# Kernel optimization log

Measured on AMD Instinct MI355X. Metric: run time of the kernel, lower is better.

## Reference

```python
import jax, jax.numpy as jnp
import numpy as np


def setup_inputs() -> dict:
    key = jax.random.key(0)
    B, F = 16384, 4096
    x = jax.random.normal(key, (B, F), dtype=jnp.float32)
    return {"x": x, "k": 64}


def reference(x, k):
    # top-k along dim=1 (last axis for 2D input)
    _, idx = jax.lax.top_k(x, k)                      # idx: [B, k]
    B = x.shape[0]
    rows = jnp.arange(B)[:, None]                     # [B, 1]
    mask = jnp.zeros_like(x).at[rows, idx].set(1.0)   # scatter ones at top-k positions
    return x * mask
```

## Files before the change

kernel.cpp:

```cpp
#include <hip/hip_runtime.h>
#include <stdint.h>

#define TK_F       4096
#define TK_THREADS 256
#define TK_EPT     16
#define TK_NBINS   2048
#define TK_HSLOTS  (TK_NBINS + (TK_NBINS >> 5))
#define TK_CAP     256

__device__ __forceinline__ unsigned int tk_f2u(unsigned int b) {
    return b ^ ((unsigned int)(((int)b) >> 31) | 0x80000000u);
}
__device__ __forceinline__ unsigned int tk_u2f(unsigned int u) {
    return u ^ ((~(unsigned int)(((int)u) >> 31)) | 0x80000000u);
}
__device__ __forceinline__ unsigned int tk_slot(unsigned int b) {
    return b + (b >> 5);
}

__global__ __launch_bounds__(TK_THREADS, 8)
void tk_topk_mask(const float* __restrict__ x, const int* __restrict__ kp,
                  float* __restrict__ out, int B)
{
    __shared__ unsigned int hist[TK_HSLOTS];
    __shared__ unsigned int cand[TK_CAP];
    __shared__ unsigned int waveTot[TK_THREADS / 64];
    __shared__ unsigned int sh_cnt;
    __shared__ int          sh_b;
    __shared__ unsigned int sh_cum;
    __shared__ unsigned int sh_T, sh_g, sh_e;

    const int tid = threadIdx.x;
    const int row = blockIdx.x;
    if (row >= B) return;
    const unsigned int k = (unsigned int)kp[0];

    const unsigned int* xr   = (const unsigned int*)(x + (size_t)row * TK_F);
    unsigned int*       orow = (unsigned int*)(out + (size_t)row * TK_F);
    const uint4*        xv   = (const uint4*)xr;

    unsigned int u[TK_EPT];
    #pragma unroll
    for (int v = 0; v < 4; ++v) {
        uint4 q = xv[tid + v * TK_THREADS];
        u[v*4+0] = tk_f2u(q.x);
        u[v*4+1] = tk_f2u(q.y);
        u[v*4+2] = tk_f2u(q.z);
        u[v*4+3] = tk_f2u(q.w);
    }

    #pragma unroll
    for (int i = 0; i < 8; ++i) hist[tid + i * TK_THREADS] = 0u;
    if (tid < TK_HSLOTS - 8 * TK_THREADS) hist[8 * TK_THREADS + tid] = 0u;
    if (tid == 0) { sh_cnt = 0u; sh_b = -1; }
    __syncthreads();

    #pragma unroll
    for (int e = 0; e < TK_EPT; ++e)
        atomicAdd(&hist[tk_slot(u[e] >> 21)], 1u);
    __syncthreads();

    unsigned int hbin[8];
    unsigned int s = 0;
    const unsigned int sbase = tk_slot((unsigned int)tid * 8u);
    #pragma unroll
    for (int j = 0; j < 8; ++j) { hbin[j] = hist[sbase + j]; s += hbin[j]; }

    unsigned int acc = s;
    const int lane = tid & 63;
    #pragma unroll
    for (int d = 1; d < 64; d <<= 1) {
        unsigned int v = (unsigned int)__shfl_down((int)acc, d, 64);
        if (lane + d < 64) acc += v;
    }
    const int wid = tid >> 6;
    if (lane == 0) waveTot[wid] = acc;
    __syncthreads();
    unsigned int later = 0;
    #pragma unroll
    for (int w = 0; w < TK_THREADS / 64; ++w)
        if (w > wid) later += waveTot[w];

    unsigned int run = later + (acc - s);
    #pragma unroll
    for (int j = 7; j >= 0; --j) {
        unsigned int h = hbin[j];
        if (run < k && run + h >= k) { sh_b = tid * 8 + j; sh_cum = run; }
        run += h;
    }
    __syncthreads();

    const int b = sh_b;
    if (b < 0) {
        #pragma unroll
        for (int v = 0; v < 4; ++v) {
            uint4 q;
            q.x = tk_u2f(u[v*4+0]); q.y = tk_u2f(u[v*4+1]);
            q.z = tk_u2f(u[v*4+2]); q.w = tk_u2f(u[v*4+3]);
            ((uint4*)orow)[tid + v * TK_THREADS] = q;
        }
        return;
    }
    const unsigned int cum = sh_cum;

    #pragma unroll
    for (int e = 0; e < TK_EPT; ++e) {
        if ((int)(u[e] >> 21) == b) {
            unsigned int p = atomicAdd(&sh_cnt, 1u);
            if (p < TK_CAP) cand[p] = u[e];
        }
    }
    __syncthreads();

    const unsigned int L = (sh_cnt < TK_CAP) ? sh_cnt : TK_CAP;
    const unsigned int r = k - cum;
    for (unsigned int j = tid; j < L; j += TK_THREADS) {
        unsigned int uj = cand[j];
        unsigned int g = 0, eq = 0;
        for (unsigned int i = 0; i < L; ++i) {
            unsigned int ui = cand[i];
            g  += (ui > uj)  ? 1u : 0u;
            eq += (ui == uj) ? 1u : 0u;
        }
        if (g < r && g + eq >= r) { sh_T = uj; sh_g = g; sh_e = eq; }
    }
    __syncthreads();

    const unsigned int T  = sh_T;
    const unsigned int re = r - sh_g;
    const unsigned int ce = sh_e;
    const bool easy = (ce == re);

    #pragma unroll
    for (int v = 0; v < 4; ++v) {
        uint4 q;
        #pragma unroll
        for (int j = 0; j < 4; ++j) {
            unsigned int uu  = u[v*4+j];
            unsigned int val = 0u;
            if (uu > T) {
                val = tk_u2f(uu);
            } else if (uu == T) {
                if (easy) {
                    val = tk_u2f(uu);
                } else {
                    int idx = (tid + v * TK_THREADS) * 4 + j;
                    unsigned int cnt = 0;
                    for (int i = 0; i < idx; ++i)
                        cnt += (tk_f2u(xr[i]) == T) ? 1u : 0u;
                    if (cnt < re) val = tk_u2f(uu);
                }
            }
            (&q.x)[j] = val;
        }
        ((uint4*)orow)[tid + v * TK_THREADS] = q;
    }
}

extern "C" void kernel_launch(void* const* d_in, const int* in_sizes, int n_in,
                              void* d_out, int out_size, void* d_ws, size_t ws_size,
                              hipStream_t stream) {
    const float* x   = (const float*)d_in[0];
    const int*   kp  = (const int*)d_in[1];
    float*       out = (float*)d_out;
    const int B = in_sizes[0] / TK_F;
    hipLaunchKernelGGL(tk_topk_mask, dim3(B), dim3(TK_THREADS), 0, stream,
                       x, kp, out, B);
}
```

Measured before the change: 527.9 us.

## Process 16 rows per persistent block with double-buffered register prefetch

Each block now handles 16 rows, alternating two register buffers so the next-next row's global load is issued while the current row is being selected. Barriers are replaced by a lighter lgkmcnt-wait plus s_barrier, the histogram is reset with vector stores, and candidate appends are aggregated per thread to cut LDS atomics. The goal is to hide HBM load latency behind the histogram and selection work. In exchange the grid is 16x smaller (1024 blocks), the register budget is higher, and launch bounds are lowered to 4 blocks per CU, which may reduce occupancy.

```diff
diff --git a/kernel.cpp b/kernel.cpp
--- a/kernel.cpp
+++ b/kernel.cpp
@@ -3,7 +3,7 @@
 
 #define TK_F       4096
 #define TK_THREADS 256
-#define TK_EPT     16
+#define TK_R       16
 #define TK_NBINS   2048
 #define TK_HSLOTS  (TK_NBINS + (TK_NBINS >> 5))
 #define TK_CAP     256
@@ -18,142 +18,198 @@
     return b + (b >> 5);
 }
 
-__global__ __launch_bounds__(TK_THREADS, 8)
+#define TK_BAR() do {                                          \
+    asm volatile("s_waitcnt lgkmcnt(0)" ::: "memory");         \
+    __builtin_amdgcn_s_barrier();                              \
+    asm volatile("" ::: "memory");                             \
+} while (0)
+
+#define TK_BODY(U, RR) do {                                                         \
+    const int  row = rowBase + (RR);                                                \
+    const bool rv  = (row < B);                                                     \
+    const size_t rbase = (size_t)(rv ? row : (B - 1)) * TK_F;                       \
+            \
+    _Pragma("unroll")                                                               \
+    for (int e = 0; e < 16; ++e) {                                                  \
+        const unsigned int uu = tk_f2u(U[e]);                                       \
+        U[e] = uu;                                                                  \
+        atomicAdd(&hist[tk_slot(uu >> 21)], 1u);                                    \
+    }                                                                               \
+    TK_BAR();                                           \
+                             \
+    unsigned int hbin[8]; unsigned int s = 0;                                       \
+    { const unsigned int sb = tk_slot((unsigned int)tid * 8u);                      \
+      _Pragma("unroll")                                                             \
+      for (int j = 0; j < 8; ++j) { hbin[j] = hist[sb + j]; s += hbin[j]; } }       \
+    unsigned int acc = s;                                                           \
+    _Pragma("unroll")                                                               \
+    for (int d = 1; d < 64; d <<= 1) {                                              \
+        const unsigned int t_ = (unsigned int)__shfl_down((int)acc, d, 64);         \
+        if (lane + d < 64) acc += t_;                                               \
+    }                                                                               \
+    if (lane == 0) ((unsigned int*)&waveTotV)[wid] = acc;                           \
+    TK_BAR();                                          \
+    { const uint4 wt = waveTotV;                                                    \
+      unsigned int later = 0;                                                       \
+      if (wid < 3) later += wt.w;                                                   \
+      if (wid < 2) later += wt.z;                                                   \
+      if (wid < 1) later += wt.y;                                                   \
+      unsigned int run = later + (acc - s);                                         \
+      _Pragma("unroll")                                                             \
+      for (int j = 7; j >= 0; --j) {                                                \
+          const unsigned int h = hbin[j];                                           \
+          if (run < k && run + h >= k) { sh_b = tid * 8 + j; sh_cum = run; }        \
+          run += h;                                                                 \
+      }                                                                             \
+      if (tid == 0) sh_cnt = 0u;  \
+    }                                                                               \
+    TK_BAR();                          \
+    {                                                                               \
+      const int          bb  = sh_b;                                                \
+      const unsigned int cum = sh_cum;                                              \
+                     \
+      unsigned int c0 = 0, c1 = 0, nm = 0;                                          \
+      _Pragma("unroll")                                                             \
+      for (int e = 0; e < 16; ++e) {                                                \
+          const unsigned int uu = U[e];                                             \
+          if ((int)(uu >> 21) == bb) {                                              \
+              if (nm == 0u) c0 = uu;                                                \
+              else if (nm == 1u) c1 = uu;                                           \
+              else { const unsigned int p = atomicAdd(&sh_cnt, 1u);                 \
+                     if (p < TK_CAP) cand[p] = uu; }                                \
+              ++nm;                                                                 \
+          }                                                                         \
+      }                                                                             \
+      if (nm) {                                                                     \
+          const unsigned int take = nm < 2u ? nm : 2u;                              \
+          const unsigned int p0 = atomicAdd(&sh_cnt, take);                         \
+          if (p0 < TK_CAP) cand[p0] = c0;                                           \
+          if (take > 1u && p0 + 1u < TK_CAP) cand[p0 + 1u] = c1;                    \
+      }                                                                             \
+               \
+      const uint4 z4 = make_uint4(0u, 0u, 0u, 0u);                                  \
+      hist4[tid] = z4; hist4[tid + 256] = z4;                                       \
+      if (tid < (TK_HSLOTS / 4 - 512)) hist4[512 + tid] = z4;                       \
+      TK_BAR();                          \
+      const unsigned int L  = sh_cnt < TK_CAP ? sh_cnt : TK_CAP;                    \
+      const unsigned int rk = k - cum;                                              \
+      for (unsigned int j = (unsigned int)tid; j < L; j += TK_THREADS) {            \
+          const unsigned int uj = cand[j];                                          \
+          unsigned int g = 0, eq = 0;                                               \
+          for (unsigned int i = 0; i < L; ++i) {                                    \
+              const unsigned int ui = cand[i];                                      \
+              g  += (ui > uj)  ? 1u : 0u;                                           \
+              eq += (ui == uj) ? 1u : 0u;                                           \
+          }                                                                         \
+          if (g < rk && g + eq >= rk) { sh_T = uj; sh_g = g; sh_e = eq; }           \
+      }                                                                             \
+      TK_BAR();                                          \
+      const unsigned int T  = sh_T;                                                 \
+      const unsigned int re = rk - sh_g;                                            \
+      const bool easy = (sh_e == re);                                               \
+      unsigned int*       orow = (unsigned int*)(out + rbase);                      \
+      const unsigned int* xr   = (const unsigned int*)(x + rbase);                  \
+      _Pragma("unroll")                                                             \
+      for (int v = 0; v < 4; ++v) {                                                 \
+          uint4 q;                                                                  \
+          _Pragma("unroll")                                                         \
+          for (int j = 0; j < 4; ++j) {                                             \
+              const unsigned int uu = U[v*4 + j];                                   \
+              unsigned int val = 0u;                                                \
+              if (uu > T) {                                                         \
+                  val = tk_u2f(uu);                                                 \
+              } else if (uu == T) {                                                 \
+                  if (easy) { val = tk_u2f(uu); }                                   \
+                  else {                                                            \
+                             \
+                      const int idx = (tid + v * TK_THREADS) * 4 + j;               \
+                      unsigned int c2 = 0;                                          \
+                      for (int i = 0; i < idx; ++i)                                 \
+                          c2 += (tk_f2u(xr[i]) == T) ? 1u : 0u;                     \
+                      if (c2 < re) val = tk_u2f(uu);                                \
+                  }                                                                 \
+              }                                                                     \
+              (&q.x)[j] = val;                                                      \
+          }                                                                         \
+          if (rv) ((uint4*)orow)[tid + v * TK_THREADS] = q;                         \
+      }                                                                             \
+            \
+      if ((RR) + 2 < TK_R) {                                                        \
+          int prow = rowBase + (RR) + 2; if (prow >= B) prow = B - 1;               \
+          const uint4* pv = (const uint4*)(x + (size_t)prow * TK_F);                \
+          _Pragma("unroll")                                                         \
+          for (int v = 0; v < 4; ++v) {                                             \
+              const uint4 q = pv[tid + v * TK_THREADS];                             \
+              U[v*4+0] = q.x; U[v*4+1] = q.y; U[v*4+2] = q.z; U[v*4+3] = q.w;       \
+          }                                                                         \
+      }                                                                             \
+    }                                                                               \
+} while (0)
+
+__global__ __launch_bounds__(TK_THREADS, 4)
 void tk_topk_mask(const float* __restrict__ x, const int* __restrict__ kp,
                   float* __restrict__ out, int B)
 {
-    __shared__ unsigned int hist[TK_HSLOTS];
+    __shared__ uint4        hist4[TK_HSLOTS / 4];
     __shared__ unsigned int cand[TK_CAP];
-    __shared__ unsigned int waveTot[TK_THREADS / 64];
+    __shared__ uint4        waveTotV;
     __shared__ unsigned int sh_cnt;
     __shared__ int          sh_b;
-    __shared__ unsigned int sh_cum;
-    __shared__ unsigned int sh_T, sh_g, sh_e;
-
-    const int tid = threadIdx.x;
-    const int row = blockIdx.x;
-    if (row >= B) return;
+    __shared__ unsigned int sh_cum, sh_T, sh_g, sh_e;
+
+    const int tid  = (int)threadIdx.x;
+    const int lane = tid & 63;
+    const int wid  = tid >> 6;
+    const int rowBase = (int)blockIdx.x * TK_R;
+    if (rowBase >= B) return;
     const unsigned int k = (unsigned int)kp[0];
-
-    const unsigned int* xr   = (const unsigned int*)(x + (size_t)row * TK_F);
-    unsigned int*       orow = (unsigned int*)(out + (size_t)row * TK_F);
-    const uint4*        xv   = (const uint4*)xr;
-
-    unsigned int u[TK_EPT];
-    #pragma unroll
-    for (int v = 0; v < 4; ++v) {
-        uint4 q = xv[tid + v * TK_THREADS];
-        u[v*4+0] = tk_f2u(q.x);
-        u[v*4+1] = tk_f2u(q.y);
-        u[v*4+2] = tk_f2u(q.z);
-        u[v*4+3] = tk_f2u(q.w);
-    }
-
-    #pragma unroll
-    for (int i = 0; i < 8; ++i) hist[tid + i * TK_THREADS] = 0u;
-    if (tid < TK_HSLOTS - 8 * TK_THREADS) hist[8 * TK_THREADS + tid] = 0u;
-    if (tid == 0) { sh_cnt = 0u; sh_b = -1; }
-    __syncthreads();
-
-    #pragma unroll
-    for (int e = 0; e < TK_EPT; ++e)
-        atomicAdd(&hist[tk_slot(u[e] >> 21)], 1u);
-    __syncthreads();
-
-    unsigned int hbin[8];
-    unsigned int s = 0;
-    const unsigned int sbase = tk_slot((unsigned int)tid * 8u);
-    #pragma unroll
-    for (int j = 0; j < 8; ++j) { hbin[j] = hist[sbase + j]; s += hbin[j]; }
-
-    unsigned int acc = s;
-    const int lane = tid & 63;
-    #pragma unroll
-    for (int d = 1; d < 64; d <<= 1) {
-        unsigned int v = (unsigned int)__shfl_down((int)acc, d, 64);
-        if (lane + d < 64) acc += v;
-    }
-    const int wid = tid >> 6;
-    if (lane == 0) waveTot[wid] = acc;
-    __syncthreads();
-    unsigned int later = 0;
-    #pragma unroll
-    for (int w = 0; w < TK_THREADS / 64; ++w)
-        if (w > wid) later += waveTot[w];
-
-    unsigned int run = later + (acc - s);
-    #pragma unroll
-    for (int j = 7; j >= 0; --j) {
-        unsigned int h = hbin[j];
-        if (run < k && run + h >= k) { sh_b = tid * 8 + j; sh_cum = run; }
-        run += h;
-    }
-    __syncthreads();
-
-    const int b = sh_b;
-    if (b < 0) {
+    unsigned int* hist = (unsigned int*)hist4;
+
+    if (k == 0u || k >= TK_F) {
+        for (int r = 0; r < TK_R; ++r) {
+            const int row = rowBase + r;
+            if (row >= B) break;
+            const uint4* xv = (const uint4*)(x + (size_t)row * TK_F);
+            uint4*       ov = (uint4*)(out + (size_t)row * TK_F);
+            #pragma unroll
+            for (int v = 0; v < 4; ++v) {
+                uint4 q = make_uint4(0u, 0u, 0u, 0u);
+                if (k) q = xv[tid + v * TK_THREADS];
+                ov[tid + v * TK_THREADS] = q;
+            }
+        }
+        return;
+    }
+
+    {
+        const uint4 z4 = make_uint4(0u, 0u, 0u, 0u);
+        hist4[tid] = z4; hist4[tid + 256] = z4;
+        if (tid < (TK_HSLOTS / 4 - 512)) hist4[512 + tid] = z4;
+        if (tid == 0) sh_cnt = 0u;
+    }
+    unsigned int uA[16], uB[16];
+    {
+        int r0 = rowBase;             if (r0 >= B) r0 = B - 1;
+        int r1 = rowBase + 1;         if (r1 >= B) r1 = B - 1;
+        const uint4* p0 = (const uint4*)(x + (size_t)r0 * TK_F);
+        const uint4* p1 = (const uint4*)(x + (size_t)r1 * TK_F);
         #pragma unroll
         for (int v = 0; v < 4; ++v) {
-            uint4 q;
-            q.x = tk_u2f(u[v*4+0]); q.y = tk_u2f(u[v*4+1]);
-            q.z = tk_u2f(u[v*4+2]); q.w = tk_u2f(u[v*4+3]);
-            ((uint4*)orow)[tid + v * TK_THREADS] = q;
+            const uint4 qa = p0[tid + v * TK_THREADS];
+            uA[v*4+0] = qa.x; uA[v*4+1] = qa.y; uA[v*4+2] = qa.z; uA[v*4+3] = qa.w;
         }
-        return;
-    }
-    const unsigned int cum = sh_cum;
+        #pragma unroll
+        for (int v = 0; v < 4; ++v) {
+            const uint4 qb = p1[tid + v * TK_THREADS];
+            uB[v*4+0] = qb.x; uB[v*4+1] = qb.y; uB[v*4+2] = qb.z; uB[v*4+3] = qb.w;
+        }
+    }
+    TK_BAR();
 
     #pragma unroll
-    for (int e = 0; e < TK_EPT; ++e) {
-        if ((int)(u[e] >> 21) == b) {
-            unsigned int p = atomicAdd(&sh_cnt, 1u);
-            if (p < TK_CAP) cand[p] = u[e];
-        }
-    }
-    __syncthreads();
-
-    const unsigned int L = (sh_cnt < TK_CAP) ? sh_cnt : TK_CAP;
-    const unsigned int r = k - cum;
-    for (unsigned int j = tid; j < L; j += TK_THREADS) {
-        unsigned int uj = cand[j];
-        unsigned int g = 0, eq = 0;
-        for (unsigned int i = 0; i < L; ++i) {
-            unsigned int ui = cand[i];
-            g  += (ui > uj)  ? 1u : 0u;
-            eq += (ui == uj) ? 1u : 0u;
-        }
-        if (g < r && g + eq >= r) { sh_T = uj; sh_g = g; sh_e = eq; }
-    }
-    __syncthreads();
-
-    const unsigned int T  = sh_T;
-    const unsigned int re = r - sh_g;
-    const unsigned int ce = sh_e;
-    const bool easy = (ce == re);
-
-    #pragma unroll
-    for (int v = 0; v < 4; ++v) {
-        uint4 q;
-        #pragma unroll
-        for (int j = 0; j < 4; ++j) {
-            unsigned int uu  = u[v*4+j];
-            unsigned int val = 0u;
-            if (uu > T) {
-                val = tk_u2f(uu);
-            } else if (uu == T) {
-                if (easy) {
-                    val = tk_u2f(uu);
-                } else {
-                    int idx = (tid + v * TK_THREADS) * 4 + j;
-                    unsigned int cnt = 0;
-                    for (int i = 0; i < idx; ++i)
-                        cnt += (tk_f2u(xr[i]) == T) ? 1u : 0u;
-                    if (cnt < re) val = tk_u2f(uu);
-                }
-            }
-            (&q.x)[j] = val;
-        }
-        ((uint4*)orow)[tid + v * TK_THREADS] = q;
+    for (int rr = 0; rr < TK_R; rr += 2) {
+        TK_BODY(uA, rr);
+        TK_BODY(uB, rr + 1);
     }
 }
 
@@ -164,6 +220,6 @@
     const int*   kp  = (const int*)d_in[1];
     float*       out = (float*)d_out;
     const int B = in_sizes[0] / TK_F;
-    hipLaunchKernelGGL(tk_topk_mask, dim3(B), dim3(TK_THREADS), 0, stream,
-                       x, kp, out, B);
-}
+    hipLaunchKernelGGL(tk_topk_mask, dim3((B + TK_R - 1) / TK_R), dim3(TK_THREADS),
+                       0, stream, x, kp, out, B);
+}
```

Measured after the change: 597.4 us. 13.2% more time.
